# Optimization experiments

Measured on AMD Instinct MI355X. Metric: run time of the kernel, lower is better.

Reference implementation:

```python
import jax, jax.numpy as jnp
import numpy as np

D = 2048      # attn_dim
H = 16        # num_heads
HD = D // H   # head_dim = 128
FF = 8192     # ffn_dim
BASE = 10000.0
EPS = 1e-6


def setup_inputs() -> dict:
    key = jax.random.key(0)
    ks = jax.random.split(key, 10)
    b, t = 2, 2048
    s = 1.0 / np.sqrt(D)
    x = jax.random.normal(ks[0], (b, t, D), dtype=jnp.float32)
    position_ids = jnp.arange(b * t, dtype=jnp.int64).reshape(b, t)  # values < maxlen=4096
    return {
        "x": x,
        "position_ids": position_ids,
        "Wq": jax.random.normal(ks[1], (D, D), jnp.float32) * s,
        "Wk": jax.random.normal(ks[2], (D, D), jnp.float32) * s,
        "Wv": jax.random.normal(ks[3], (D, D), jnp.float32) * s,
        "Wo": jax.random.normal(ks[4], (D, D), jnp.float32) * s,
        "Wg": jax.random.normal(ks[5], (D, FF), jnp.float32) * s,
        "Wu": jax.random.normal(ks[6], (D, FF), jnp.float32) * s,
        "Wd": jax.random.normal(ks[7], (FF, D), jnp.float32) * (1.0 / np.sqrt(FF)),
        "g1": jnp.ones((D,), jnp.float32),
        "g2": jnp.ones((D,), jnp.float32),
    }


def _rmsnorm(x, g):
    return x * jax.lax.rsqrt(jnp.mean(x * x, axis=-1, keepdims=True) + EPS) * g


def _rope_cos_sin(position_ids):
    # get_cos_sin: theta over even dims, then repeat(1, 2) -> (b, t, HD)
    inv_freq = 1.0 / (BASE ** (jnp.arange(0, HD, 2, dtype=jnp.float32) / HD))
    ang = position_ids[..., None].astype(jnp.float32) * inv_freq  # (b, t, HD/2)
    cos = jnp.concatenate([jnp.cos(ang), jnp.cos(ang)], axis=-1)  # (b, t, HD)
    sin = jnp.concatenate([jnp.sin(ang), jnp.sin(ang)], axis=-1)
    return cos, sin


def _rotate_half(x):
    x1, x2 = x[..., : HD // 2], x[..., HD // 2:]
    return jnp.concatenate([-x2, x1], axis=-1)


def _attention(xn, position_ids, Wq, Wk, Wv, Wo):
    b, t, _ = xn.shape
    q = (xn @ Wq).reshape(b, t, H, HD).transpose(0, 2, 1, 3)  # b h t d
    k = (xn @ Wk).reshape(b, t, H, HD).transpose(0, 2, 1, 3)
    v = (xn @ Wv).reshape(b, t, H, HD).transpose(0, 2, 1, 3)
    cos, sin = _rope_cos_sin(position_ids)
    cos = cos[:, None]  # b 1 t d
    sin = sin[:, None]
    q = q * cos + _rotate_half(q) * sin
    k = k * cos + _rotate_half(k) * sin
    scores = jnp.einsum("bhqd,bhkd->bhqk", q, k) / np.sqrt(HD).astype(np.float32)
    causal = jnp.triu(jnp.ones((t, t), dtype=bool), k=1)  # True above diagonal
    scores = jnp.where(causal, jnp.float32(-10000.0), scores)
    attn = jax.nn.softmax(scores, axis=-1)
    o = jnp.einsum("bhqk,bhkd->bhqd", attn, v)
    o = o.transpose(0, 2, 1, 3).reshape(b, t, D)
    return o @ Wo


def reference(x, position_ids, Wq, Wk, Wv, Wo, Wg, Wu, Wd, g1, g2):
    x = x + _attention(_rmsnorm(x, g1), position_ids, Wq, Wk, Wv, Wo)
    h = _rmsnorm(x, g2)
    x = x + (jax.nn.silu(h @ Wg) * (h @ Wu)) @ Wd
    return x
```

## Files before the change

kernel.cpp:

```cpp
#include <hip/hip_runtime.h>
#include <cstdint>

#define D_  2048
#define H_  16
#define HD_ 128
#define FF_ 8192
#define T_  2048
#define B_  2
#define BT_ (B_*T_)
#define NP_ (B_*H_)
#define QKVLD_ (3*D_)

typedef __attribute__((ext_vector_type(8))) _Float16 half8;
typedef __attribute__((ext_vector_type(4))) float   floatx4;

__device__ __forceinline__ void gl_lds16(const void* g, void* l) {
  __builtin_amdgcn_global_load_lds(
      (const __attribute__((address_space(1))) void*)(uintptr_t)g,
      (__attribute__((address_space(3))) void*)(uintptr_t)l,
      16, 0, 0);
}

__global__ void wconv_kernel(const float* __restrict__ W, _Float16* __restrict__ Wt,
                             int K, int N) {
  __shared__ float tile[64][33];
  int n0 = blockIdx.x * 32, k0 = blockIdx.y * 64;
  int tx = threadIdx.x, ty = threadIdx.y;
#pragma unroll
  for (int r = 0; r < 64; r += 8)
    tile[ty + r][tx] = W[(size_t)(k0 + ty + r) * N + n0 + tx];
  __syncthreads();
#pragma unroll
  for (int r = 0; r < 32; r += 8) {
    float a = tile[tx * 2][ty + r], b = tile[tx * 2 + 1][ty + r];
    union { _Float16 h[2]; unsigned u; } cv;
    cv.h[0] = (_Float16)a; cv.h[1] = (_Float16)b;
    ((unsigned*)(Wt + (size_t)(n0 + ty + r) * K + k0))[tx] = cv.u;
  }
}

__global__ void rmsnorm_kernel(const float* __restrict__ x, const float* __restrict__ g,
                               _Float16* __restrict__ out) {
  int row = blockIdx.x, tid = threadIdx.x;
  const float4* xr = (const float4*)(x + (size_t)row * D_);
  float4 v1 = xr[tid], v2 = xr[tid + 256];
  float ss = v1.x*v1.x + v1.y*v1.y + v1.z*v1.z + v1.w*v1.w
           + v2.x*v2.x + v2.y*v2.y + v2.z*v2.z + v2.w*v2.w;
  __shared__ float red[256];
  red[tid] = ss; __syncthreads();
  for (int s = 128; s > 0; s >>= 1) { if (tid < s) red[tid] += red[tid + s]; __syncthreads(); }
  float rs = rsqrtf(red[0] * (1.0f / D_) + 1e-6f);
  float4 ga = ((const float4*)g)[tid], gb = ((const float4*)g)[tid + 256];
  _Float16* orow = out + (size_t)row * D_;
  _Float16 t[4] __attribute__((aligned(8)));
  t[0] = (_Float16)(v1.x * rs * ga.x);
  t[1] = (_Float16)(v1.y * rs * ga.y);
  t[2] = (_Float16)(v1.z * rs * ga.z);
  t[3] = (_Float16)(v1.w * rs * ga.w);
  *(uint2*)(orow + tid * 4) = *(const uint2*)t;
  t[0] = (_Float16)(v2.x * rs * gb.x);
  t[1] = (_Float16)(v2.y * rs * gb.y);
  t[2] = (_Float16)(v2.z * rs * gb.z);
  t[3] = (_Float16)(v2.w * rs * gb.w);
  *(uint2*)(orow + (tid + 256) * 4) = *(const uint2*)t;
}

template<int OUTMODE>
__global__ __launch_bounds__(512, 2) void gemm256(
    const _Float16* __restrict__ A, const _Float16* __restrict__ Bt,
    void* __restrict__ Cv, const float* __restrict__ Res,
    int M, int N, int K, int lda, int ldb, int ldc)
{
  extern __shared__ _Float16 smem[];

  const int gx = gridDim.x, gy = gridDim.y, gz = gridDim.z;
  int pid = (blockIdx.z * gy + blockIdx.y) * gx + blockIdx.x;
  const int qch = (gx * gy * gz) >> 3;
  int lid = (pid & 7) * qch + (pid >> 3);
  const int bx = lid % gx; lid /= gx;
  const int by = lid % gy; const int bz = lid / gy;

  const int tid  = threadIdx.x;
  const int lane = tid & 63;
  const int w    = tid >> 6;
  const int wm   = w >> 2;
  const int wn   = w & 3;
  const int l15  = lane & 15, q4 = lane >> 4;
  const int m0   = by * 256;
  const int n0   = bx * 256;
  const int KP   = K / gz;
  const int koff = bz * KP;
  const int NT   = KP >> 6;

  const int srow8  = lane >> 3;
  const int schunk = (((lane & 7) ^ (srow8 & 7)) << 3);
  const _Float16* AgP = A  + (size_t)(m0 + w * 8 + srow8) * lda + schunk + koff;
  const _Float16* BgP = Bt + (size_t)(n0 + w * 8 + srow8) * ldb + schunk + koff;
  const int ldsW = w * 512;

  const int c0 = ((q4 ^ (l15 & 7)) << 3);
  const int c1 = c0 ^ 32;
  const int arow_e = (wm * 128 + l15) * 64;
  const int brow_e = (wn * 64 + l15) * 64;
  const _Float16* aB[2][2];
  const _Float16* bB[2][2];
  aB[0][0] = smem + arow_e + c0;          aB[0][1] = smem + arow_e + c1;
  aB[1][0] = aB[0][0] + 32768;            aB[1][1] = aB[0][1] + 32768;
  bB[0][0] = smem + 16384 + brow_e + c0;  bB[0][1] = smem + 16384 + brow_e + c1;
  bB[1][0] = bB[0][0] + 32768;            bB[1][1] = bB[0][1] + 32768;

  floatx4 acc[8][4];
#pragma unroll
  for (int i = 0; i < 8; ++i)
#pragma unroll
    for (int j = 0; j < 4; ++j)
#pragma unroll
      for (int r = 0; r < 4; ++r) acc[i][j][r] = 0.0f;

  half8 bf[2][4];
  half8 af0[4], af1[4];

#define STA(S, h, s, KO)                                                     \
  gl_lds16(AgP + (size_t)((h) * 128 + (s) * 64) * lda + (KO),                \
           smem + (S) * 32768 + (h) * 8192 + (s) * 4096 + ldsW)
#define STB(S, h, s, KO)                                                     \
  gl_lds16(BgP + (size_t)((h) * 128 + (s) * 64) * ldb + (KO),                \
           smem + (S) * 32768 + 16384 + (h) * 8192 + (s) * 4096 + ldsW)

#define SB0   __builtin_amdgcn_sched_barrier(0)
#define BARR  __builtin_amdgcn_s_barrier()
#define LGKM0 asm volatile("s_waitcnt lgkmcnt(0)" ::: "memory")

#define RD_B8(S)                                                             \
  { _Pragma("unroll")                                                        \
    for (int j = 0; j < 4; ++j) {                                            \
      bf[0][j] = *(const half8*)(bB[S][0] + j * 1024);                       \
      bf[1][j] = *(const half8*)(bB[S][1] + j * 1024);                       \
    } }
#define RD_A4(S, q, af)                                                      \
  { _Pragma("unroll")                                                        \
    for (int i2 = 0; i2 < 2; ++i2) {                                         \
      af[i2*2+0] = *(const half8*)(aB[S][0] + ((q)*2+i2) * 1024);            \
      af[i2*2+1] = *(const half8*)(aB[S][1] + ((q)*2+i2) * 1024);            \
    } }
#define MFMA_Q(q, af)                                                        \
  { _Pragma("unroll")                                                        \
    for (int kk = 0; kk < 2; ++kk)                                           \
      _Pragma("unroll")                                                      \
      for (int i2 = 0; i2 < 2; ++i2)                                         \
        _Pragma("unroll")                                                    \
        for (int j = 0; j < 4; ++j)                                          \
          acc[(q)*2+i2][j] = __builtin_amdgcn_mfma_f32_16x16x32_f16(         \
              af[i2*2+kk], bf[kk][j], acc[(q)*2+i2][j], 0, 0, 0);            \
  }

#define TILE(S, t, KOA, KOB)                                                 \
  {                                                                          \
    const bool s1 = (t) + 1 < NT, s2 = (t) + 2 < NT;                         \
                                                   \
    RD_B8(S); RD_A4(S, 0, af0);                                              \
    if (s1) { STA((S) ^ 1, 0, 0, KOA); STA((S) ^ 1, 0, 1, KOA); }            \
    asm volatile("s_waitcnt lgkmcnt(8)" ::: "memory");                       \
    SB0; BARR; LGKM0; SB0;                                                   \
    __builtin_amdgcn_s_setprio(1); MFMA_Q(0, af0); __builtin_amdgcn_s_setprio(0); \
    SB0; BARR;                                                               \
                                                           \
    RD_A4(S, 1, af1);                                                        \
    if (s1) { STA((S) ^ 1, 1, 0, KOA); STA((S) ^ 1, 1, 1, KOA); }            \
    SB0; BARR; LGKM0; SB0;                                                   \
    __builtin_amdgcn_s_setprio(1); MFMA_Q(1, af1); __builtin_amdgcn_s_setprio(0); \
    SB0; BARR;                                                               \
                                                           \
    RD_A4(S, 2, af0);                                                        \
    if (s2) { STB(S, 0, 0, KOB); STB(S, 0, 1, KOB); }                        \
    SB0; BARR; LGKM0; SB0;                                                   \
    __builtin_amdgcn_s_setprio(1); MFMA_Q(2, af0); __builtin_amdgcn_s_setprio(0); \
    SB0; BARR;                                                               \
                                                           \
    RD_A4(S, 3, af1);                                                        \
    if (s2) { STB(S, 1, 0, KOB); STB(S, 1, 1, KOB); }                        \
    SB0; BARR; LGKM0; SB0;                                                   \
    __builtin_amdgcn_s_setprio(1); MFMA_Q(3, af1); __builtin_amdgcn_s_setprio(0); \
    SB0;                                                                     \
    if (s2)      asm volatile("s_waitcnt vmcnt(4)" ::: "memory");            \
    else if (s1) asm volatile("s_waitcnt vmcnt(0)" ::: "memory");            \
    BARR;                                                                    \
  }

  STA(0, 0, 0, 0); STA(0, 0, 1, 0); STA(0, 1, 0, 0); STA(0, 1, 1, 0);
  STB(0, 0, 0, 0); STB(0, 0, 1, 0); STB(0, 1, 0, 0); STB(0, 1, 1, 0);
  if (NT > 1) {
    STB(1, 0, 0, 64); STB(1, 0, 1, 64); STB(1, 1, 0, 64); STB(1, 1, 1, 64);
    asm volatile("s_waitcnt vmcnt(4)" ::: "memory");
  } else {
    asm volatile("s_waitcnt vmcnt(0)" ::: "memory");
  }
  BARR;

  for (int t = 0; t < NT; t += 2) {
    TILE(0, t,     64, 128);
    TILE(1, t + 1, 128, 192);
    AgP += 128; BgP += 128;
  }

#undef STA
#undef STB
#undef SB0
#undef BARR
#undef LGKM0
#undef RD_B8
#undef RD_A4
#undef MFMA_Q
#undef TILE

  const int crow0 = m0 + wm * 128 + q4 * 4;
  const int ccol0 = n0 + wn * 64 + l15;
#pragma unroll
  for (int i = 0; i < 8; ++i)
#pragma unroll
    for (int j = 0; j < 4; ++j)
#pragma unroll
      for (int r = 0; r < 4; ++r) {
        size_t o = (size_t)(crow0 + i * 16 + r) * ldc + (ccol0 + j * 16);
        if constexpr (OUTMODE == 0)      ((_Float16*)Cv)[o] = (_Float16)acc[i][j][r];
        else if constexpr (OUTMODE == 1) ((float*)Cv)[o] = acc[i][j][r] + Res[o];
        else ((float*)Cv)[(size_t)bz * M * ldc + o] = acc[i][j][r];
      }
}

__global__ void addred_kernel(const float* __restrict__ parts, const float* __restrict__ res,
                              float* __restrict__ out) {
  size_t i = ((size_t)blockIdx.x * 256 + threadIdx.x) * 4;
  const size_t MN = (size_t)BT_ * D_;
  float4 a = *(const float4*)(parts + i);
  float4 b = *(const float4*)(parts + MN + i);
  float4 r = *(const float4*)(res + i);
  float4 o;
  o.x = a.x + b.x + r.x; o.y = a.y + b.y + r.y;
  o.z = a.z + b.z + r.z; o.w = a.w + b.w + r.w;
  *(float4*)(out + i) = o;
}

__global__ __launch_bounds__(256, 2) void fattn_kernel(
    const _Float16* __restrict__ qkv, const _Float16* __restrict__ vt,
    _Float16* __restrict__ ob)
{
  __shared__ _Float16 Pl[128 * 136];
  const int pr = blockIdx.x;
  const int yq = blockIdx.y;
  const int qb = (yq < 8) ? yq : 23 - yq;
  const int b = pr >> 4, h = pr & 15;
  const int lane = threadIdx.x & 63, w = threadIdx.x >> 6;
  const int l15 = lane & 15, q4 = lane >> 4;
  const float scale = 0.08838834764831845f;

  const _Float16* qg = qkv + (size_t)b * T_ * QKVLD_ + (size_t)h * HD_;
  const _Float16* kg = qg + D_;
  const _Float16* vg = vt + (size_t)pr * HD_ * T_;
  _Float16* og = ob + (size_t)b * T_ * D_ + (size_t)h * HD_;

  const int qrow0 = qb * 128 + w * 32;

  half8 qf[2][4];
#pragma unroll
  for (int i = 0; i < 2; ++i)
#pragma unroll
    for (int kf = 0; kf < 4; ++kf)
      qf[i][kf] = *(const half8*)(qg + (size_t)(qrow0 + i * 16 + l15) * QKVLD_
                                     + kf * 32 + q4 * 8);

  floatx4 Oa[2][8];
  float m[8], l[8];
#pragma unroll
  for (int i = 0; i < 2; ++i)
#pragma unroll
    for (int j = 0; j < 8; ++j)
#pragma unroll
      for (int r = 0; r < 4; ++r) Oa[i][j][r] = 0.f;
#pragma unroll
  for (int z = 0; z < 8; ++z) { m[z] = -1e30f; l[z] = 0.f; }

  for (int kt = 0; kt <= qb; ++kt) {
    const _Float16* kb_ = kg + (size_t)(kt * 128 + l15) * QKVLD_ + q4 * 8;
    half8 k0[8], k1[8];
#pragma unroll
    for (int j = 0; j < 8; ++j)
      k0[j] = *(const half8*)(kb_ + (size_t)(j * 16) * QKVLD_);
    floatx4 s[2][8];
#pragma unroll
    for (int i = 0; i < 2; ++i)
#pragma unroll
      for (int j = 0; j < 8; ++j)
#pragma unroll
        for (int r = 0; r < 4; ++r) s[i][j][r] = 0.f;
#pragma unroll
    for (int kf = 0; kf < 4; ++kf) {
      if (kf < 3) {
#pragma unroll
        for (int j = 0; j < 8; ++j) {
          half8 nx = *(const half8*)(kb_ + (size_t)(j * 16) * QKVLD_ + (kf + 1) * 32);
          if (kf & 1) k0[j] = nx; else k1[j] = nx;
        }
      }
#pragma unroll
      for (int j = 0; j < 8; ++j) {
        half8 cur = (kf & 1) ? k1[j] : k0[j];
        s[0][j] = __builtin_amdgcn_mfma_f32_16x16x32_f16(qf[0][kf], cur, s[0][j], 0, 0, 0);
        s[1][j] = __builtin_amdgcn_mfma_f32_16x16x32_f16(qf[1][kf], cur, s[1][j], 0, 0, 0);
      }
    }
#pragma unroll
    for (int i = 0; i < 2; ++i)
#pragma unroll
      for (int j = 0; j < 8; ++j)
#pragma unroll
        for (int r = 0; r < 4; ++r) s[i][j][r] *= scale;
    if (kt == qb) {
#pragma unroll
      for (int i = 0; i < 2; ++i)
#pragma unroll
        for (int j = 0; j < 8; ++j)
#pragma unroll
          for (int r = 0; r < 4; ++r)
            if (j * 16 + l15 > w * 32 + i * 16 + q4 * 4 + r) s[i][j][r] = -1e30f;
    }
    const _Float16* vb_ = vg + (size_t)(l15) * T_ + kt * 128 + q4 * 8;
    half8 v0[8], v1[8];
#pragma unroll
    for (int jd = 0; jd < 8; ++jd)
      v0[jd] = *(const half8*)(vb_ + (size_t)(jd * 16) * T_);
#pragma unroll
    for (int i = 0; i < 2; ++i)
#pragma unroll
      for (int r = 0; r < 4; ++r) {
        const int z = i * 4 + r;
        float pm = s[i][0][r];
#pragma unroll
        for (int j = 1; j < 8; ++j) pm = fmaxf(pm, s[i][j][r]);
        pm = fmaxf(pm, __shfl_xor(pm, 1));
        pm = fmaxf(pm, __shfl_xor(pm, 2));
        pm = fmaxf(pm, __shfl_xor(pm, 4));
        pm = fmaxf(pm, __shfl_xor(pm, 8));
        float mn = fmaxf(m[z], pm);
        float sc = __expf(m[z] - mn);
        m[z] = mn;
        float ls = 0.f;
#pragma unroll
        for (int j = 0; j < 8; ++j) {
          float e = __expf(s[i][j][r] - mn);
          s[i][j][r] = e;
          ls += e;
        }
        ls += __shfl_xor(ls, 1);
        ls += __shfl_xor(ls, 2);
        ls += __shfl_xor(ls, 4);
        ls += __shfl_xor(ls, 8);
        l[z] = l[z] * sc + ls;
#pragma unroll
        for (int jd = 0; jd < 8; ++jd) Oa[i][jd][r] *= sc;
      }
#pragma unroll
    for (int i = 0; i < 2; ++i)
#pragma unroll
      for (int r = 0; r < 4; ++r) {
        _Float16* prow = &Pl[(size_t)(w * 32 + i * 16 + q4 * 4 + r) * 136 + l15];
#pragma unroll
        for (int j = 0; j < 8; ++j) prow[j * 16] = (_Float16)s[i][j][r];
      }
#pragma unroll
    for (int ks = 0; ks < 4; ++ks) {
      if (ks < 3) {
#pragma unroll
        for (int jd = 0; jd < 8; ++jd) {
          half8 nx = *(const half8*)(vb_ + (size_t)(jd * 16) * T_ + (ks + 1) * 32);
          if (ks & 1) v0[jd] = nx; else v1[jd] = nx;
        }
      }
      half8 pf0 = *(const half8*)&Pl[(size_t)(w * 32 + l15) * 136 + ks * 32 + q4 * 8];
      half8 pf1 = *(const half8*)&Pl[(size_t)(w * 32 + 16 + l15) * 136 + ks * 32 + q4 * 8];
#pragma unroll
      for (int jd = 0; jd < 8; ++jd) {
        half8 vf = (ks & 1) ? v1[jd] : v0[jd];
        Oa[0][jd] = __builtin_amdgcn_mfma_f32_16x16x32_f16(pf0, vf, Oa[0][jd], 0, 0, 0);
        Oa[1][jd] = __builtin_amdgcn_mfma_f32_16x16x32_f16(pf1, vf, Oa[1][jd], 0, 0, 0);
      }
    }
  }
#pragma unroll
  for (int i = 0; i < 2; ++i)
#pragma unroll
    for (int r = 0; r < 4; ++r) {
      float inv = 1.0f / l[i * 4 + r];
      _Float16* orow = og + (size_t)(qrow0 + i * 16 + q4 * 4 + r) * D_;
#pragma unroll
      for (int jd = 0; jd < 8; ++jd)
        orow[jd * 16 + l15] = (_Float16)(Oa[i][jd][r] * inv);
    }
}

__global__ void rope_kernel(_Float16* __restrict__ qkv, const void* __restrict__ pos) {
  int gid = blockIdx.x * 256 + threadIdx.x;
  int d = gid & 63;
  int h = (gid >> 6) & 15;
  int bt = gid >> 10;
  const int* pi = (const int*)pos;
  long long pv = (pi[1] == 0 && pi[2] == 1) ? ((const long long*)pos)[bt]
                                            : (long long)pi[bt];
  float inv = exp2f((float)d * -0.2076205059304601f);
  float ang = (float)pv * inv;
  float s, c;
  sincosf(ang, &s, &c);
  size_t base = (size_t)bt * QKVLD_ + (size_t)h * HD_ + d;
  _Float16* q = qkv;
  _Float16* k = qkv + D_;
  float x1v = (float)q[base], x2v = (float)q[base + 64];
  q[base]      = (_Float16)(x1v * c - x2v * s);
  q[base + 64] = (_Float16)(x2v * c + x1v * s);
  x1v = (float)k[base]; x2v = (float)k[base + 64];
  k[base]      = (_Float16)(x1v * c - x2v * s);
  k[base + 64] = (_Float16)(x2v * c + x1v * s);
}

__global__ void vtrans_kernel(const _Float16* __restrict__ v, _Float16* __restrict__ vt,
                              int ld) {
  __shared__ _Float16 tile[32][33];
  int t0 = blockIdx.x * 32, d0 = blockIdx.y * 32, bh = blockIdx.z;
  int b = bh >> 4, h = bh & 15;
  int tx = threadIdx.x, ty = threadIdx.y;
  const _Float16* vb = v + (size_t)b * T_ * ld + (size_t)h * HD_;
#pragma unroll
  for (int r = 0; r < 32; r += 8)
    tile[ty + r][tx] = vb[(size_t)(t0 + ty + r) * ld + d0 + tx];
  __syncthreads();
  _Float16* vo = vt + ((size_t)bh * HD_ + d0) * T_ + t0;
#pragma unroll
  for (int r = 0; r < 32; r += 8)
    vo[(size_t)(ty + r) * T_ + tx] = tile[tx][ty + r];
}

__global__ void silumul_kernel(_Float16* __restrict__ gate, const _Float16* __restrict__ up) {
  size_t idx = ((size_t)blockIdx.x * 256 + threadIdx.x) * 8;
  uint4 gr = *(const uint4*)(gate + idx);
  uint4 ur = *(const uint4*)(up + idx);
  const _Float16* gh = (const _Float16*)&gr;
  const _Float16* uh = (const _Float16*)&ur;
  _Float16 t[8] __attribute__((aligned(16)));
#pragma unroll
  for (int l = 0; l < 8; l++) {
    float x = (float)gh[l];
    float s = x / (1.0f + __expf(-x));
    t[l] = (_Float16)(s * (float)uh[l]);
  }
  *(uint4*)(gate + idx) = *(const uint4*)t;
}

extern "C" void kernel_launch(void* const* d_in, const int* in_sizes, int n_in,
                              void* d_out, int out_size, void* d_ws, size_t ws_size,
                              hipStream_t stream) {
  (void)in_sizes; (void)n_in; (void)out_size;
  const float* x   = (const float*)d_in[0];
  const void*  pos = d_in[1];
  const float* W[7] = { (const float*)d_in[2], (const float*)d_in[3],
                        (const float*)d_in[4], (const float*)d_in[5],
                        (const float*)d_in[6], (const float*)d_in[7],
                        (const float*)d_in[8] };
  const float* g1  = (const float*)d_in[9];
  const float* g2  = (const float*)d_in[10];
  float* out = (float*)d_out;

  const int wk[7] = { D_, D_, D_, D_, D_, D_, FF_ };
  const int wn[7] = { D_, D_, D_, D_, FF_, FF_, D_ };

  char* p = (char*)d_ws;
  auto carve = [&](size_t bytes) { char* r = p; p += (bytes + 255) & ~(size_t)255; return r; };

  _Float16* scratch = (_Float16*)carve((size_t)64 * 1024 * 1024);
  const size_t FLAT_NEED = (size_t)336 * 1024 * 1024;
  bool flat = ws_size >= FLAT_NEED;
  _Float16* w16[7];
  if (flat) {
    for (int i = 0; i < 7; i++) w16[i] = (_Float16*)carve((size_t)wk[i] * wn[i] * 2);
  } else {
    _Float16* wslot = (_Float16*)carve((size_t)D_ * FF_ * 2);
    w16[0] = wslot;
    w16[1] = wslot + (size_t)D_ * D_;
    w16[2] = wslot + (size_t)2 * D_ * D_;
    w16[3] = w16[4] = w16[5] = w16[6] = wslot;
  }
  _Float16* qkv = (_Float16*)carve((size_t)BT_ * QKVLD_ * 2);
  _Float16* ob  = (_Float16*)carve((size_t)BT_ * D_ * 2);
  _Float16* xn  = (_Float16*)carve((size_t)BT_ * D_ * 2);
  _Float16* vt  = (_Float16*)carve((size_t)BT_ * D_ * 2);
  float*    x1  = (float*)   carve((size_t)BT_ * D_ * 4);
  _Float16* gate = scratch;
  _Float16* up   = qkv;
  _Float16* hb   = xn;
  float* oparts = (float*)scratch;
  float* dparts = (float*)qkv;

  dim3 b328(32, 8);
  auto conv = [&](int i) {
    wconv_kernel<<<dim3(wn[i] / 32, wk[i] / 64), b328, 0, stream>>>(W[i], w16[i], wk[i], wn[i]);
  };
  if (flat) for (int i = 0; i < 7; i++) conv(i);

  rmsnorm_kernel<<<BT_, 256, 0, stream>>>(x, g1, xn);

  if (!flat) { conv(0); conv(1); conv(2); }
  gemm256<0><<<dim3(QKVLD_ / 256, BT_ / 256, 1), 512, 131072, stream>>>(
      xn, w16[0], qkv, nullptr, BT_, QKVLD_, D_, D_, D_, QKVLD_);

  rope_kernel<<<(BT_ * H_ * 64) / 256, 256, 0, stream>>>(qkv, pos);

  vtrans_kernel<<<dim3(T_ / 32, HD_ / 32, NP_), b328, 0, stream>>>(qkv + 2 * D_, vt, QKVLD_);

  fattn_kernel<<<dim3(NP_, 16), 256, 0, stream>>>(qkv, vt, ob);

  if (!flat) conv(3);
  gemm256<2><<<dim3(D_ / 256, BT_ / 256, 2), 512, 131072, stream>>>(
      ob, w16[3], oparts, nullptr, BT_, D_, D_, D_, D_, D_);
  addred_kernel<<<(BT_ * D_ / 4) / 256, 256, 0, stream>>>(oparts, x, x1);

  rmsnorm_kernel<<<BT_, 256, 0, stream>>>(x1, g2, hb);

  if (!flat) conv(4);
  gemm256<0><<<dim3(FF_ / 256, BT_ / 256, 1), 512, 131072, stream>>>(
      hb, w16[4], gate, nullptr, BT_, FF_, D_, D_, D_, FF_);
  if (!flat) conv(5);
  gemm256<0><<<dim3(FF_ / 256, BT_ / 256, 1), 512, 131072, stream>>>(
      hb, w16[5], up, nullptr, BT_, FF_, D_, D_, D_, FF_);

  silumul_kernel<<<(BT_ * FF_ / 8) / 256, 256, 0, stream>>>(gate, up);

  if (!flat) conv(6);
  gemm256<2><<<dim3(D_ / 256, BT_ / 256, 2), 512, 131072, stream>>>(
      gate, w16[6], dparts, nullptr, BT_, D_, FF_, FF_, FF_, D_);
  addred_kernel<<<(BT_ * D_ / 4) / 256, 256, 0, stream>>>(dparts, x1, out);
}
```

Before: 1.134 ms.

## Split flash attention KV range across two blocks and merge partial results

Flash attention now splits each query block's causal key range into two halves handled by separate blocks (grid z=2). Each half writes unnormalized fp32 partial outputs plus per-row max and sum, and a new merge kernel combines them with log-sum-exp rescaling into the fp16 output. The aim is more parallelism and better load balance across CUs, and K tile loads are also prefetched across iterations. The cost is extra fp32 partial traffic, a second kernel launch, and empty-half blocks that write zeros.

```diff
diff --git a/kernel.cpp b/kernel.cpp
--- a/kernel.cpp
+++ b/kernel.cpp
@@ -243,22 +243,39 @@
 
 __global__ __launch_bounds__(256, 2) void fattn_kernel(
     const _Float16* __restrict__ qkv, const _Float16* __restrict__ vt,
-    _Float16* __restrict__ ob)
+    float* __restrict__ opart, float* __restrict__ mlb)
 {
   __shared__ _Float16 Pl[128 * 136];
   const int pr = blockIdx.x;
   const int yq = blockIdx.y;
+  const int sp = blockIdx.z;
   const int qb = (yq < 8) ? yq : 23 - yq;
+  const int nt = qb + 1;
+  const int nh = (nt + 1) >> 1;
+  const int lo = sp ? nh : 0;
+  const int hi = sp ? nt : nh;
   const int b = pr >> 4, h = pr & 15;
   const int lane = threadIdx.x & 63, w = threadIdx.x >> 6;
   const int l15 = lane & 15, q4 = lane >> 4;
   const float scale = 0.08838834764831845f;
 
+  float* og  = opart + ((size_t)(sp * 32 + pr) * T_ + (size_t)qb * 128) * 128;
+  float* mlg = mlb   + ((size_t)(sp * 32 + pr) * T_ + (size_t)qb * 128) * 2;
+
+  if (lo >= hi) {
+    float4 z4 = {0.f, 0.f, 0.f, 0.f};
+    for (int idx = threadIdx.x; idx < 128 * 128 / 4; idx += 256)
+      *(float4*)(og + (size_t)idx * 4) = z4;
+    if (threadIdx.x < 128) {
+      mlg[threadIdx.x * 2]     = -1e30f;
+      mlg[threadIdx.x * 2 + 1] = 0.f;
+    }
+    return;
+  }
+
   const _Float16* qg = qkv + (size_t)b * T_ * QKVLD_ + (size_t)h * HD_;
   const _Float16* kg = qg + D_;
   const _Float16* vg = vt + (size_t)pr * HD_ * T_;
-  _Float16* og = ob + (size_t)b * T_ * D_ + (size_t)h * HD_;
-
   const int qrow0 = qb * 128 + w * 32;
 
   half8 qf[2][4];
@@ -280,12 +297,17 @@
 #pragma unroll
   for (int z = 0; z < 8; ++z) { m[z] = -1e30f; l[z] = 0.f; }
 
-  for (int kt = 0; kt <= qb; ++kt) {
+  half8 k0[8], k1[8];
+  {
+    const _Float16* kp = kg + (size_t)(lo * 128 + l15) * QKVLD_ + q4 * 8;
+#pragma unroll
+    for (int j = 0; j < 8; ++j)
+      k0[j] = *(const half8*)(kp + (size_t)(j * 16) * QKVLD_);
+  }
+
+  for (int kt = lo; kt < hi; ++kt) {
     const _Float16* kb_ = kg + (size_t)(kt * 128 + l15) * QKVLD_ + q4 * 8;
-    half8 k0[8], k1[8];
-#pragma unroll
-    for (int j = 0; j < 8; ++j)
-      k0[j] = *(const half8*)(kb_ + (size_t)(j * 16) * QKVLD_);
+    const _Float16* kn_ = kg + (size_t)((kt + 1) * 128 + l15) * QKVLD_ + q4 * 8;
     floatx4 s[2][8];
 #pragma unroll
     for (int i = 0; i < 2; ++i)
@@ -301,6 +323,10 @@
           half8 nx = *(const half8*)(kb_ + (size_t)(j * 16) * QKVLD_ + (kf + 1) * 32);
           if (kf & 1) k0[j] = nx; else k1[j] = nx;
         }
+      } else if (kt + 1 < hi) {
+#pragma unroll
+        for (int j = 0; j < 8; ++j)
+          k0[j] = *(const half8*)(kn_ + (size_t)(j * 16) * QKVLD_);
       }
 #pragma unroll
       for (int j = 0; j < 8; ++j) {
@@ -386,16 +412,50 @@
       }
     }
   }
+  float* ogw = og + (size_t)(w * 32) * 128;
 #pragma unroll
   for (int i = 0; i < 2; ++i)
 #pragma unroll
     for (int r = 0; r < 4; ++r) {
-      float inv = 1.0f / l[i * 4 + r];
-      _Float16* orow = og + (size_t)(qrow0 + i * 16 + q4 * 4 + r) * D_;
+      const int rr = i * 16 + q4 * 4 + r;
+      float* orow = ogw + (size_t)rr * 128;
 #pragma unroll
       for (int jd = 0; jd < 8; ++jd)
-        orow[jd * 16 + l15] = (_Float16)(Oa[i][jd][r] * inv);
+        orow[jd * 16 + l15] = Oa[i][jd][r];
+      if (l15 == 0) {
+        mlg[(size_t)(w * 32 + rr) * 2]     = m[i * 4 + r];
+        mlg[(size_t)(w * 32 + rr) * 2 + 1] = l[i * 4 + r];
+      }
     }
+}
+
+__global__ void fmerge_kernel(const float* __restrict__ op, const float* __restrict__ mlb,
+                              _Float16* __restrict__ ob) {
+  int gid = blockIdx.x * 256 + threadIdx.x;
+  int tc = gid & 15, rw = gid >> 4;
+  int pr = rw >> 11, trow = rw & 2047;
+  size_t r1 = (size_t)pr * T_ + trow;
+  size_t r2 = (size_t)(pr + 32) * T_ + trow;
+  float m1 = mlb[r1 * 2], l1 = mlb[r1 * 2 + 1];
+  float m2 = mlb[r2 * 2], l2 = mlb[r2 * 2 + 1];
+  float mm = fmaxf(m1, m2);
+  float e1 = __expf(m1 - mm), e2 = __expf(m2 - mm);
+  float inv = 1.0f / (l1 * e1 + l2 * e2);
+  float4 a1 = *(const float4*)(op + r1 * 128 + tc * 8);
+  float4 b1 = *(const float4*)(op + r1 * 128 + tc * 8 + 4);
+  float4 a2 = *(const float4*)(op + r2 * 128 + tc * 8);
+  float4 b2 = *(const float4*)(op + r2 * 128 + tc * 8 + 4);
+  _Float16 t8[8] __attribute__((aligned(16)));
+  t8[0] = (_Float16)((a1.x * e1 + a2.x * e2) * inv);
+  t8[1] = (_Float16)((a1.y * e1 + a2.y * e2) * inv);
+  t8[2] = (_Float16)((a1.z * e1 + a2.z * e2) * inv);
+  t8[3] = (_Float16)((a1.w * e1 + a2.w * e2) * inv);
+  t8[4] = (_Float16)((b1.x * e1 + b2.x * e2) * inv);
+  t8[5] = (_Float16)((b1.y * e1 + b2.y * e2) * inv);
+  t8[6] = (_Float16)((b1.z * e1 + b2.z * e2) * inv);
+  t8[7] = (_Float16)((b1.w * e1 + b2.w * e2) * inv);
+  int b_ = pr >> 4, h = pr & 15;
+  *(uint4*)(ob + ((size_t)b_ * T_ + trow) * D_ + h * HD_ + tc * 8) = *(const uint4*)t8;
 }
 
 __global__ void rope_kernel(_Float16* __restrict__ qkv, const void* __restrict__ pos) {
@@ -495,6 +555,8 @@
   _Float16* gate = scratch;
   _Float16* up   = qkv;
   _Float16* hb   = xn;
+  float* opart  = (float*)scratch;
+  float* mlbuf  = (float*)xn;
   float* oparts = (float*)scratch;
   float* dparts = (float*)qkv;
 
@@ -514,7 +576,8 @@
 
   vtrans_kernel<<<dim3(T_ / 32, HD_ / 32, NP_), b328, 0, stream>>>(qkv + 2 * D_, vt, QKVLD_);
 
-  fattn_kernel<<<dim3(NP_, 16), 256, 0, stream>>>(qkv, vt, ob);
+  fattn_kernel<<<dim3(NP_, 16, 2), 256, 0, stream>>>(qkv, vt, opart, mlbuf);
+  fmerge_kernel<<<(NP_ * T_ * 16) / 256, 256, 0, stream>>>(opart, mlbuf, ob);
 
   if (!flat) conv(3);
   gemm256<2><<<dim3(D_ / 256, BT_ / 256, 2), 512, 131072, stream>>>(
```

After: 1.222 ms. +7.7%, slower.

## Pre-pack K and V into MFMA fragment order for coalesced attention loads

Applied to the files above, without the earlier changes.

Replaces the V transpose kernel with two packing kernels that rearrange K and V into per-lane MFMA fragment order, so each wave's 16-byte loads in the flash-attention inner loop become contiguous 1KB chunks instead of strided row reads. This targets uncoalesced global loads of K (stride 3*D) and V in the attention kernel. It adds an extra pass over K and reuses the xn buffer as K-pack storage, which is safe only because xn is not needed again until rmsnorm rewrites it.

```diff
diff --git a/kernel.cpp b/kernel.cpp
--- a/kernel.cpp
+++ b/kernel.cpp
@@ -241,9 +241,57 @@
   *(float4*)(out + i) = o;
 }
 
+__global__ void kpack_kernel(const _Float16* __restrict__ qkv, _Float16* __restrict__ kp) {
+  __shared__ _Float16 tile[32][40];
+  int t0 = blockIdx.x * 32, d0 = blockIdx.y * 32, bh = blockIdx.z;
+  int b = bh >> 4, h = bh & 15;
+  int tx = threadIdx.x, ty = threadIdx.y;
+  const _Float16* kb = qkv + (size_t)b * T_ * QKVLD_ + D_ + (size_t)h * HD_;
+#pragma unroll
+  for (int r = 0; r < 32; r += 8)
+    tile[ty + r][tx] = kb[(size_t)(t0 + ty + r) * QKVLD_ + d0 + tx];
+  __syncthreads();
+  int tid = ty * 32 + tx;
+  if (tid < 128) {
+    int tt = tid & 31;
+    int c  = tid >> 5;
+    int t = t0 + tt, d = d0 + c * 8;
+    _Float16 v8[8] __attribute__((aligned(16)));
+#pragma unroll
+    for (int e = 0; e < 8; ++e) v8[e] = tile[tt][c * 8 + e];
+    size_t frag = ((size_t)bh * (T_ / 16) + (t >> 4)) * 4 + (d >> 5);
+    int lane = (t & 15) + (((d >> 3) & 3) << 4);
+    *(uint4*)(kp + frag * 512 + lane * 8) = *(const uint4*)v8;
+  }
+}
+
+__global__ void vpack_kernel(const _Float16* __restrict__ qkv, _Float16* __restrict__ vp) {
+  __shared__ _Float16 tile[32][40];
+  int t0 = blockIdx.x * 32, d0 = blockIdx.y * 32, bh = blockIdx.z;
+  int b = bh >> 4, h = bh & 15;
+  int tx = threadIdx.x, ty = threadIdx.y;
+  const _Float16* vb = qkv + (size_t)b * T_ * QKVLD_ + 2 * D_ + (size_t)h * HD_;
+#pragma unroll
+  for (int r = 0; r < 32; r += 8)
+    tile[ty + r][tx] = vb[(size_t)(t0 + ty + r) * QKVLD_ + d0 + tx];
+  __syncthreads();
+  int tid = ty * 32 + tx;
+  if (tid < 128) {
+    int dd = tid & 31;
+    int tg = tid >> 5;
+    int d = d0 + dd, t = t0 + tg * 8;
+    _Float16 v8[8] __attribute__((aligned(16)));
+#pragma unroll
+    for (int e = 0; e < 8; ++e) v8[e] = tile[tg * 8 + e][dd];
+    size_t frag = (((size_t)bh * 16 + (t >> 7)) * 4 + ((t >> 5) & 3)) * 8 + (d >> 4);
+    int lane = (d & 15) + (((t >> 3) & 3) << 4);
+    *(uint4*)(vp + frag * 512 + lane * 8) = *(const uint4*)v8;
+  }
+}
+
 __global__ __launch_bounds__(256, 2) void fattn_kernel(
-    const _Float16* __restrict__ qkv, const _Float16* __restrict__ vt,
-    _Float16* __restrict__ ob)
+    const _Float16* __restrict__ qkv, const _Float16* __restrict__ kp,
+    const _Float16* __restrict__ vp, _Float16* __restrict__ ob)
 {
   __shared__ _Float16 Pl[128 * 136];
   const int pr = blockIdx.x;
@@ -255,9 +303,9 @@
   const float scale = 0.08838834764831845f;
 
   const _Float16* qg = qkv + (size_t)b * T_ * QKVLD_ + (size_t)h * HD_;
-  const _Float16* kg = qg + D_;
-  const _Float16* vg = vt + (size_t)pr * HD_ * T_;
   _Float16* og = ob + (size_t)b * T_ * D_ + (size_t)h * HD_;
+  const _Float16* kpp = kp + (size_t)pr * 128 * 4 * 512 + lane * 8;
+  const _Float16* vpp = vp + (size_t)pr * 16 * 32 * 512 + lane * 8;
 
   const int qrow0 = qb * 128 + w * 32;
 
@@ -281,11 +329,11 @@
   for (int z = 0; z < 8; ++z) { m[z] = -1e30f; l[z] = 0.f; }
 
   for (int kt = 0; kt <= qb; ++kt) {
-    const _Float16* kb_ = kg + (size_t)(kt * 128 + l15) * QKVLD_ + q4 * 8;
+    const _Float16* kT = kpp + (size_t)kt * 8 * 4 * 512;
     half8 k0[8], k1[8];
 #pragma unroll
     for (int j = 0; j < 8; ++j)
-      k0[j] = *(const half8*)(kb_ + (size_t)(j * 16) * QKVLD_);
+      k0[j] = *(const half8*)(kT + j * 2048);
     floatx4 s[2][8];
 #pragma unroll
     for (int i = 0; i < 2; ++i)
@@ -298,7 +346,7 @@
       if (kf < 3) {
 #pragma unroll
         for (int j = 0; j < 8; ++j) {
-          half8 nx = *(const half8*)(kb_ + (size_t)(j * 16) * QKVLD_ + (kf + 1) * 32);
+          half8 nx = *(const half8*)(kT + j * 2048 + (kf + 1) * 512);
           if (kf & 1) k0[j] = nx; else k1[j] = nx;
         }
       }
@@ -324,11 +372,11 @@
           for (int r = 0; r < 4; ++r)
             if (j * 16 + l15 > w * 32 + i * 16 + q4 * 4 + r) s[i][j][r] = -1e30f;
     }
-    const _Float16* vb_ = vg + (size_t)(l15) * T_ + kt * 128 + q4 * 8;
+    const _Float16* vT = vpp + (size_t)kt * 32 * 512;
     half8 v0[8], v1[8];
 #pragma unroll
     for (int jd = 0; jd < 8; ++jd)
-      v0[jd] = *(const half8*)(vb_ + (size_t)(jd * 16) * T_);
+      v0[jd] = *(const half8*)(vT + jd * 512);
 #pragma unroll
     for (int i = 0; i < 2; ++i)
 #pragma unroll
@@ -372,7 +420,7 @@
       if (ks < 3) {
 #pragma unroll
         for (int jd = 0; jd < 8; ++jd) {
-          half8 nx = *(const half8*)(vb_ + (size_t)(jd * 16) * T_ + (ks + 1) * 32);
+          half8 nx = *(const half8*)(vT + ((ks + 1) * 8 + jd) * 512);
           if (ks & 1) v0[jd] = nx; else v1[jd] = nx;
         }
       }
@@ -421,23 +469,6 @@
   k[base + 64] = (_Float16)(x2v * c + x1v * s);
 }
 
-__global__ void vtrans_kernel(const _Float16* __restrict__ v, _Float16* __restrict__ vt,
-                              int ld) {
-  __shared__ _Float16 tile[32][33];
-  int t0 = blockIdx.x * 32, d0 = blockIdx.y * 32, bh = blockIdx.z;
-  int b = bh >> 4, h = bh & 15;
-  int tx = threadIdx.x, ty = threadIdx.y;
-  const _Float16* vb = v + (size_t)b * T_ * ld + (size_t)h * HD_;
-#pragma unroll
-  for (int r = 0; r < 32; r += 8)
-    tile[ty + r][tx] = vb[(size_t)(t0 + ty + r) * ld + d0 + tx];
-  __syncthreads();
-  _Float16* vo = vt + ((size_t)bh * HD_ + d0) * T_ + t0;
-#pragma unroll
-  for (int r = 0; r < 32; r += 8)
-    vo[(size_t)(ty + r) * T_ + tx] = tile[tx][ty + r];
-}
-
 __global__ void silumul_kernel(_Float16* __restrict__ gate, const _Float16* __restrict__ up) {
   size_t idx = ((size_t)blockIdx.x * 256 + threadIdx.x) * 8;
   uint4 gr = *(const uint4*)(gate + idx);
@@ -495,6 +526,8 @@
   _Float16* gate = scratch;
   _Float16* up   = qkv;
   _Float16* hb   = xn;
+  _Float16* kpb  = xn;
+  _Float16* vpb  = vt;
   float* oparts = (float*)scratch;
   float* dparts = (float*)qkv;
 
@@ -512,9 +545,10 @@
 
   rope_kernel<<<(BT_ * H_ * 64) / 256, 256, 0, stream>>>(qkv, pos);
 
-  vtrans_kernel<<<dim3(T_ / 32, HD_ / 32, NP_), b328, 0, stream>>>(qkv + 2 * D_, vt, QKVLD_);
-
-  fattn_kernel<<<dim3(NP_, 16), 256, 0, stream>>>(qkv, vt, ob);
+  kpack_kernel<<<dim3(T_ / 32, HD_ / 32, NP_), b328, 0, stream>>>(qkv, kpb);
+  vpack_kernel<<<dim3(T_ / 32, HD_ / 32, NP_), b328, 0, stream>>>(qkv, vpb);
+
+  fattn_kernel<<<dim3(NP_, 16), 256, 0, stream>>>(qkv, kpb, vpb, ob);
 
   if (!flat) conv(3);
   gemm256<2><<<dim3(D_ / 256, BT_ / 256, 2), 512, 131072, stream>>>(
```

Measured after the change: 1.088 ms. -4.1%, faster.
